# Performance work log

Measured on AMD Instinct MI355X. Metric: run time of the kernel, lower is better.

## Reference

```python
import jax, jax.numpy as jnp
import numpy as np

DIM = 1024
HEAD_DIM = 64
NUM_HEADS = DIM // HEAD_DIM
SCALE = HEAD_DIM ** -0.5
B, N, M = 2, 1024, 2048


def setup_inputs() -> dict:
    key = jax.random.key(0)
    ks = jax.random.split(key, 7)
    x = jax.random.normal(ks[0], (B, N, DIM), dtype=jnp.float32)
    context = jax.random.normal(ks[1], (B, M, DIM), dtype=jnp.float32)
    # query row has at least one valid key (avoids all -inf softmax rows).
    mask = jax.random.bernoulli(ks[2], 0.9, (B, N, M))
    mask = mask.at[:, :, 0].set(True)
    # Linear params (torch nn.Linear convention: y = x @ W.T + b)
    sq = (1.0 / DIM) ** 0.5
    Wq = jax.random.uniform(ks[3], (DIM, DIM), minval=-sq, maxval=sq, dtype=jnp.float32)
    Wkv = jax.random.uniform(ks[4], (2 * DIM, DIM), minval=-sq, maxval=sq, dtype=jnp.float32)
    b_kv = jax.random.uniform(ks[5], (2 * DIM,), minval=-sq, maxval=sq, dtype=jnp.float32)
    Wo = jax.random.uniform(ks[6], (DIM, DIM), minval=-sq, maxval=sq, dtype=jnp.float32)
    return {"x": x, "context": context, "mask": mask,
            "Wq": Wq, "Wkv": Wkv, "b_kv": b_kv, "Wo": Wo}


def reference(x, context, mask, Wq, Wkv, b_kv, Wo):
    b, n, c = x.shape
    m = context.shape[1]
    h, d = NUM_HEADS, HEAD_DIM
    # Q projection (no bias): [b, n, h, d] -> bhnd
    q = (x @ Wq.T).reshape(b, n, h, d).transpose(0, 2, 1, 3)
    # KV projection (with bias): [b, m, 2, h, d]
    kv = (context @ Wkv.T + b_kv).reshape(b, m, 2, h, d)
    k = kv[:, :, 0].transpose(0, 2, 1, 3)  # bhmd
    v = kv[:, :, 1].transpose(0, 2, 1, 3)  # bhmd
    # scores: bhnm, scale applied after matmul as in the original
    attn = jnp.einsum('bhnd,bhmd->bhnm', q, k) * SCALE
    attn = jnp.where(mask[:, None, :, :], attn, -jnp.inf)
    attn = jax.nn.softmax(attn, axis=-1)
    out = jnp.einsum('bhnm,bhmd->bhnd', attn, v)
    out = out.transpose(0, 2, 1, 3).reshape(b, n, h * d)
    return out @ Wo.T
```

## Files before the change

kernel.cpp:

```cpp
#include <hip/hip_runtime.h>


typedef __attribute__((ext_vector_type(8))) short short8;
typedef __attribute__((ext_vector_type(4))) short short4v;
typedef __attribute__((ext_vector_type(4))) float f32x4;
typedef __attribute__((ext_vector_type(4))) int int4v;

#define SCL2E 0.18033688011112042592f

__device__ __forceinline__ float bf2f(short s) {
  unsigned u = ((unsigned)(unsigned short)s) << 16;
  return __uint_as_float(u);
}
__device__ __forceinline__ short f2bf(float f) {
  unsigned u = __float_as_uint(f);
  u += 0x7fffu + ((u >> 16) & 1u);
  return (short)(u >> 16);
}
__device__ __forceinline__ int cvt_pk_bf16(float a, float b) {
  int r;
  asm("v_cvt_pk_bf16_f32 %0, %1, %2" : "=v"(r) : "v"(a), "v"(b));
  return r;
}
__device__ __forceinline__ void gld_lds16(const void* gp, void* lp) {
  __builtin_amdgcn_global_load_lds(
      (const __attribute__((address_space(1))) unsigned int*)gp,
      (__attribute__((address_space(3))) unsigned int*)lp, 16, 0, 0);
}
__device__ __forceinline__ void sbar() {
  __builtin_amdgcn_sched_barrier(0);
  __builtin_amdgcn_s_barrier();
  __builtin_amdgcn_sched_barrier(0);
}
#define WAITVM(N) asm volatile("s_waitcnt vmcnt(" #N ")" ::: "memory")

__device__ __forceinline__ void pipesync() {
  asm volatile("s_waitcnt vmcnt(0) lgkmcnt(0)" ::: "memory");
  __builtin_amdgcn_sched_barrier(0);
  __builtin_amdgcn_s_barrier();
  __builtin_amdgcn_sched_barrier(0);
}
__device__ __forceinline__ short4v cvt4(float4 v) {
  short4v o;
  o[0] = f2bf(v.x); o[1] = f2bf(v.y); o[2] = f2bf(v.z); o[3] = f2bf(v.w);
  return o;
}
__device__ __forceinline__ size_t off128(int row, int k) {
  return ((size_t)(((row >> 7) * 32 + (k >> 5)) * 8 + ((row >> 4) & 7)) << 9) +
         (((((k >> 3) & 3) * 16 + (row & 15)) << 3) + (k & 7));
}
__device__ __forceinline__ size_t off64(int row, int k) {
  return ((size_t)(((row >> 6) * 32 + (k >> 5)) * 4 + ((row >> 4) & 3)) << 9) +
         (((((k >> 3) & 3) * 16 + (row & 15)) << 3) + (k & 7));
}

__global__ __launch_bounds__(256) void prep(
    const unsigned char* __restrict__ mask, unsigned long long* __restrict__ pm,
    const float* __restrict__ Wq, const float* __restrict__ Wkv,
    const float* __restrict__ Wo, const float* __restrict__ x,
    const float* __restrict__ ctx, short* __restrict__ wqb,
    short* __restrict__ wkvb, short* __restrict__ wob,
    short* __restrict__ xb, short* __restrict__ ctxb) {
  const int row = blockIdx.x;
  const int wave = threadIdx.x >> 6, lane = threadIdx.x & 63;
  const unsigned char p8 = mask[lane * 4 + 1];
  const int p32 = ((const int*)mask)[lane * 2 + 1];
  const int shift =
      (__ballot(p8 != 0) != 0ull) ? 0 : ((__ballot(p32 != 0) != 0ull) ? 2 : 3);
  const size_t mbase = ((size_t)row * 2048) << shift;
#pragma unroll
  for (int j = 0; j < 8; j++) {
    const int c = wave * 512 + j * 64 + lane;
    const unsigned long long bits = __ballot(mask[mbase + ((size_t)c << shift)] != 0);
    if (lane == 0) pm[(size_t)row * 32 + wave * 8 + j] = bits;
  }
  const int gid = blockIdx.x * 256 + threadIdx.x;
  {
    const int e = gid * 4, r = e >> 10, k = e & 1023;
    *(short4v*)(xb + off128(r, k)) = cvt4(((const float4*)x)[gid]);
  }
  {
    int e = gid * 4, r = e >> 10, k = e & 1023;
    *(short4v*)(ctxb + off128(r, k)) = cvt4(((const float4*)ctx)[gid]);
    e = (gid + 524288) * 4; r = e >> 10; k = e & 1023;
    *(short4v*)(ctxb + off128(r, k)) = cvt4(((const float4*)ctx)[gid + 524288]);
  }
  {
    const int e = gid * 4, r = e >> 10, k = e & 1023;
    *(short4v*)(wkvb + off128(r, k)) = cvt4(((const float4*)Wkv)[gid]);
  }
  if (gid < 262144) {
    const int e = gid * 4, r = e >> 10, k = e & 1023;
    *(short4v*)(wqb + off128(r, k)) = cvt4(((const float4*)Wq)[gid]);
    *(short4v*)(wob + off64(r, k)) = cvt4(((const float4*)Wo)[gid]);
  }
}

__global__ __launch_bounds__(256, 3)
void qkv_gemm(const short* __restrict__ xb, const short* __restrict__ ctxb,
              const short* __restrict__ wqb, const short* __restrict__ wkvb,
              const float* __restrict__ bias, short* __restrict__ qws,
              short* __restrict__ kws, short* __restrict__ vtws) {
  __shared__ __align__(16) short ldsA[3][4096];
  __shared__ __align__(16) short ldsB[3][4096];
  const int tid = threadIdx.x;
  const int wave = tid >> 6, lane = tid & 63;
  const int l15 = lane & 15, lg = lane >> 4;
  const int bx0 = blockIdx.x;
  const int bx = (bx0 & 7) * 80 + (bx0 >> 3);
  const bool isKV = bx < 512;
  const int rt = isKV ? (bx >> 4) : ((bx - 512) >> 3);
  const int ct = isKV ? (bx & 15) : ((bx - 512) & 7);
  const short* Amat = isKV ? ctxb : xb;
  const short* Bw = isKV ? wkvb : wqb;
  const int wr = wave >> 1, wc = wave & 1;

  f32x4 acc[4][4];
#pragma unroll
  for (int i = 0; i < 4; i++)
#pragma unroll
    for (int j = 0; j < 4; j++) acc[i][j] = (f32x4){0.f, 0.f, 0.f, 0.f};

  const short* ga0 = Amat + (size_t)rt * 131072 + wave * 512 + lane * 8;
  const short* ga1 = ga0 + 2048;
  const short* gb0 = Bw + (size_t)ct * 131072 + wave * 512 + lane * 8;
  const short* gb1 = gb0 + 2048;

  auto stage = [&](int kk, int buf) {
    const size_t koff = (size_t)kk * 4096;
    short* dA = &ldsA[buf][0];
    short* dB = &ldsB[buf][0];
    gld_lds16(ga0 + koff, dA + wave * 512);
    gld_lds16(ga1 + koff, dA + (wave + 4) * 512);
    gld_lds16(gb0 + koff, dB + wave * 512);
    gld_lds16(gb1 + koff, dB + (wave + 4) * 512);
  };
  auto compute = [&](int buf) {
    const short* sA = &ldsA[buf][0];
    const short* sB = &ldsB[buf][0];
    short8 af[4], bfr[4];
#pragma unroll
    for (int t = 0; t < 4; t++)
      af[t] = *(const short8*)&sA[((wr * 4 + t) * 64 + lane) * 8];
#pragma unroll
    for (int t = 0; t < 4; t++)
      bfr[t] = *(const short8*)&sB[((wc * 4 + t) * 64 + lane) * 8];
#pragma unroll
    for (int i = 0; i < 4; i++)
#pragma unroll
      for (int j = 0; j < 4; j++)
        acc[i][j] =
            __builtin_amdgcn_mfma_f32_16x16x32_bf16(af[i], bfr[j], acc[i][j], 0, 0, 0);
  };

  stage(0, 0);
  stage(1, 1);
  int cur = 0, nxt = 2;
  for (int i = 0; i < 30; ++i) {
    WAITVM(4);
    sbar();
    stage(i + 2, nxt);
    compute(cur);
    cur = (cur == 2) ? 0 : cur + 1;
    nxt = (nxt == 2) ? 0 : nxt + 1;
  }
  WAITVM(4);
  sbar();
  compute(cur);
  cur = (cur == 2) ? 0 : cur + 1;
  WAITVM(0);
  sbar();
  compute(cur);

#pragma unroll
  for (int i = 0; i < 4; i++)
#pragma unroll
    for (int j = 0; j < 4; j++)
#pragma unroll
      for (int r = 0; r < 4; r++) {
        const int gr = rt * 128 + wr * 64 + i * 16 + lg * 4 + r;
        const int gc = ct * 128 + wc * 64 + j * 16 + l15;
        float v = acc[i][j][r];
        if (isKV) {
          v += bias[gc];
          const int b = gr >> 11, m = gr & 2047;
          const int kv = gc >> 10, hh = (gc >> 6) & 15, d = gc & 63;
          if (kv == 0)
            kws[((((size_t)b * 16 + hh) * 2048 + m) << 6) + d] = f2bf(v);
          else {
            const int mp = (m & ~31) | (((m >> 2) & 3) << 3) |
                           (((m >> 4) & 1) << 2) | (m & 3);
            vtws[(((size_t)b * 16 + hh) * 64 + d) * 2048 + mp] = f2bf(v);
          }
        } else {
          const int b = gr >> 10, n = gr & 1023, hh = gc >> 6, d = gc & 63;
          qws[((((size_t)b * 16 + hh) * 1024 + n) << 6) + d] = f2bf(v * SCL2E);
        }
      }
}

__global__ __launch_bounds__(512, 4)
void attn_split(const short* __restrict__ Qg, const short* __restrict__ Kg,
                const short* __restrict__ Vtg,
                const unsigned int* __restrict__ pm,
                float* __restrict__ opart, float* __restrict__ lpart) {
  __shared__ __align__(16) short ldsK[2][8192];
  __shared__ __align__(16) short ldsV[2][8192];
  const int tid = threadIdx.x;
  const int w = tid >> 6, lane = tid & 63;
  const int l15 = lane & 15, lg = lane >> 4;
  const int bx = blockIdx.x;
  const int bhid = bx & 31, qt = (bx >> 5) & 7, half = bx >> 8;
  const int b = bhid >> 4, h = bhid & 15;
  const int n0 = qt * 128, m_base = half * 1024;
  const size_t bh = (size_t)b * 16 + h;
  const short* Qb = Qg + (bh * 1024 + n0) * 64;
  const short* Kb = Kg + (bh << 17);
  const short* Vb = Vtg + (bh << 17);
  const unsigned int* pmw =
      pm + ((size_t)(b * 1024 + n0 + w * 16 + l15) << 6) + (m_base >> 5);

  auto stageKV = [&](int c, short* dK, short* dV) {
    const int m0 = m_base + c * 128;
#pragma unroll
    for (int ii = 0; ii < 2; ii++) {
      const int f = w * 2 + ii;
      const int t = f >> 1, ks = f & 1;
      gld_lds16(Kb + (size_t)(m0 + t * 16 + l15) * 64 + ks * 32 + lg * 8,
                dK + f * 512);
      const int vt = f >> 2, vk = f & 3;
      gld_lds16(Vb + (size_t)(vt * 16 + l15) * 2048 + (m0 + vk * 32 + lg * 8),
                dV + f * 512);
    }
  };

#pragma unroll
  for (int ii = 0; ii < 2; ii++)
    gld_lds16(Qb + (size_t)(w * 16 + l15) * 64 + ii * 32 + lg * 8,
              &ldsK[0][(w * 2 + ii) * 512]);
  stageKV(0, ldsK[1], ldsV[1]);
  pipesync();
  short8 qf[2];
#pragma unroll
  for (int ks = 0; ks < 2; ks++)
    qf[ks] = *(const short8*)&ldsK[0][((w * 2 + ks) * 64 + lane) * 8];
  asm volatile("s_waitcnt lgkmcnt(0)" ::: "memory");
  __builtin_amdgcn_sched_barrier(0);
  __builtin_amdgcn_s_barrier();
  __builtin_amdgcn_sched_barrier(0);

  short8 onesf;
#pragma unroll
  for (int i = 0; i < 8; i++) onesf[i] = (short)0x3F80;

  f32x4 o[4], lacc;
#pragma unroll
  for (int ct = 0; ct < 4; ct++) o[ct] = (f32x4){0.f, 0.f, 0.f, 0.f};
  lacc = (f32x4){0.f, 0.f, 0.f, 0.f};
  const int sb = lg * 4;

  auto computeC = [&](int c, const short* sK, const short* sV) {
    const uint4 mk = *(const uint4*)(pmw + c * 4);
    int4v pw4[4];
#pragma unroll
    for (int h2 = 0; h2 < 2; h2++) {
      f32x4 s[4];
#pragma unroll
      for (int t2 = 0; t2 < 4; t2++) s[t2] = (f32x4){0.f, 0.f, 0.f, 0.f};
#pragma unroll
      for (int t2 = 0; t2 < 4; t2++) {
        const int t = h2 * 4 + t2;
#pragma unroll
        for (int ks = 0; ks < 2; ks++) {
          const short8 kf = *(const short8*)&sK[((t * 2 + ks) * 64 + lane) * 8];
          s[t2] = __builtin_amdgcn_mfma_f32_16x16x32_bf16(kf, qf[ks], s[t2], 0, 0, 0);
        }
      }
#pragma unroll
      for (int t2 = 0; t2 < 4; t2++) {
        const int t = h2 * 4 + t2;
        const unsigned int mw = ((t >> 1) == 0) ? mk.x
                              : ((t >> 1) == 1) ? mk.y
                              : ((t >> 1) == 2) ? mk.z : mk.w;
        float p[4];
#pragma unroll
        for (int r = 0; r < 4; r++) {
          const bool att = (mw >> (((t & 1) << 4) + sb + r)) & 1;
          p[r] = exp2f(att ? s[t2][r] : -1e30f);
        }
        pw4[t >> 1][(t & 1) * 2] = cvt_pk_bf16(p[0], p[1]);
        pw4[t >> 1][(t & 1) * 2 + 1] = cvt_pk_bf16(p[2], p[3]);
      }
    }
#pragma unroll
    for (int ks2 = 0; ks2 < 4; ks2++) {
      const short8 pf = __builtin_bit_cast(short8, pw4[ks2]);
#pragma unroll
      for (int ct = 0; ct < 4; ct++) {
        const short8 vf = *(const short8*)&sV[((ct * 4 + ks2) * 64 + lane) * 8];
        o[ct] = __builtin_amdgcn_mfma_f32_16x16x32_bf16(pf, vf, o[ct], 0, 0, 0);
      }
      lacc = __builtin_amdgcn_mfma_f32_16x16x32_bf16(pf, onesf, lacc, 0, 0, 0);
    }
  };

  for (int c = 0; c < 8; c += 2) {
    if (c + 1 < 8) stageKV(c + 1, ldsK[0], ldsV[0]);
    computeC(c, ldsK[1], ldsV[1]);
    pipesync();
    if (c + 2 < 8) stageKV(c + 2, ldsK[1], ldsV[1]);
    computeC(c + 1, ldsK[0], ldsV[0]);
    pipesync();
  }

#pragma unroll
  for (int ct = 0; ct < 4; ct++)
#pragma unroll
    for (int r = 0; r < 4; r++) {
      const int n = n0 + w * 16 + lg * 4 + r;
      opart[((size_t)half << 21) + (((size_t)b * 1024 + n) << 10) + h * 64 +
            ct * 16 + l15] = o[ct][r];
    }
  if (l15 == 0) {
#pragma unroll
    for (int r = 0; r < 4; r++) {
      const int n = n0 + w * 16 + lg * 4 + r;
      lpart[((size_t)half << 15) + bh * 1024 + n] = lacc[r];
    }
  }
}

__global__ __launch_bounds__(256) void combine(
    const float* __restrict__ opart, const float* __restrict__ lpart,
    short* __restrict__ aoT) {
  const int gid = blockIdx.x * 256 + threadIdx.x;
  const size_t base = (size_t)gid * 4;
  const int row = (int)(base >> 10), col = (int)(base & 1023);
  const int b = row >> 10, n = row & 1023, h = col >> 6;
  const float4 o1 = *(const float4*)(opart + base);
  const float4 o2 = *(const float4*)(opart + (1u << 21) + base);
  const float l1 = lpart[(size_t)(b * 16 + h) * 1024 + n];
  const float l2 = lpart[(1u << 15) + (size_t)(b * 16 + h) * 1024 + n];
  const float inv = 1.f / fmaxf(l1 + l2, 1e-30f);
  short4v o;
  o[0] = f2bf((o1.x + o2.x) * inv); o[1] = f2bf((o1.y + o2.y) * inv);
  o[2] = f2bf((o1.z + o2.z) * inv); o[3] = f2bf((o1.w + o2.w) * inv);
  *(short4v*)(aoT + off64(row, col)) = o;
}

__global__ __launch_bounds__(256, 2)
void o_gemm(const short* __restrict__ aoT, const short* __restrict__ wobT,
            float* __restrict__ Of) {
  __shared__ __align__(16) short ldsA[3][2048];
  __shared__ __align__(16) short ldsB[3][2048];
  const int tid = threadIdx.x;
  const int w = tid >> 6, lane = tid & 63;
  const int l15 = lane & 15, lg = lane >> 4;
  const int bx0 = blockIdx.x;
  const int bx = (bx0 & 7) * 64 + (bx0 >> 3);
  const int rt = bx >> 4, ct = bx & 15;

  f32x4 acc[4];
#pragma unroll
  for (int j = 0; j < 4; j++) acc[j] = (f32x4){0.f, 0.f, 0.f, 0.f};

  const short* ga = aoT + (size_t)rt * 65536 + w * 512 + lane * 8;
  const short* gb = wobT + (size_t)ct * 65536 + w * 512 + lane * 8;

  auto stage = [&](int kk, int buf) {
    const size_t koff = (size_t)kk * 2048;
    gld_lds16(ga + koff, &ldsA[buf][0] + w * 512);
    gld_lds16(gb + koff, &ldsB[buf][0] + w * 512);
  };
  auto compute = [&](int buf) {
    const short* sA = &ldsA[buf][0];
    const short* sB = &ldsB[buf][0];
    const short8 af = *(const short8*)&sA[(w * 64 + lane) * 8];
#pragma unroll
    for (int j = 0; j < 4; j++) {
      const short8 bf = *(const short8*)&sB[(j * 64 + lane) * 8];
      acc[j] = __builtin_amdgcn_mfma_f32_16x16x32_bf16(af, bf, acc[j], 0, 0, 0);
    }
  };

  stage(0, 0);
  stage(1, 1);
  int cur = 0, nxt = 2;
  for (int i = 0; i < 30; ++i) {
    WAITVM(2);
    sbar();
    stage(i + 2, nxt);
    compute(cur);
    cur = (cur == 2) ? 0 : cur + 1;
    nxt = (nxt == 2) ? 0 : nxt + 1;
  }
  WAITVM(2);
  sbar();
  compute(cur);
  cur = (cur == 2) ? 0 : cur + 1;
  WAITVM(0);
  sbar();
  compute(cur);

#pragma unroll
  for (int j = 0; j < 4; j++)
#pragma unroll
    for (int r = 0; r < 4; r++) {
      const int gr = rt * 64 + w * 16 + lg * 4 + r;
      const int gc = ct * 64 + j * 16 + l15;
      Of[(size_t)gr * 1024 + gc] = acc[j][r];
    }
}

extern "C" void kernel_launch(void* const* d_in, const int* in_sizes, int n_in,
                              void* d_out, int out_size, void* d_ws, size_t ws_size,
                              hipStream_t stream) {
  const float* x   = (const float*)d_in[0];
  const float* ctx = (const float*)d_in[1];
  const unsigned char* mask = (const unsigned char*)d_in[2];
  const float* Wq  = (const float*)d_in[3];
  const float* Wkv = (const float*)d_in[4];
  const float* bkv = (const float*)d_in[5];
  const float* Wo  = (const float*)d_in[6];
  float* out = (float*)d_out;

  char* wsb = (char*)d_ws;
  short* qws  = (short*)(wsb);
  short* kws  = (short*)(wsb + (4u << 20));
  short* vtws = (short*)(wsb + (12u << 20));
  short* wqb  = (short*)(wsb + (20u << 20));
  short* wkvb = (short*)(wsb + (22u << 20));
  short* wob  = (short*)(wsb + (26u << 20));
  unsigned long long* pmws = (unsigned long long*)(wsb + (28u << 20));
  float* opart = (float*)(wsb + (29u << 20));
  float* lpart = (float*)(wsb + (45u << 20));
  short* xb   = (short*)(wsb + (29u << 20));
  short* ctxb = (short*)(wsb + (33u << 20));
  short* ao = (short*)(wsb + (20u << 20));

  prep<<<2048, 256, 0, stream>>>(mask, pmws, Wq, Wkv, Wo, x, ctx,
                                 wqb, wkvb, wob, xb, ctxb);
  qkv_gemm<<<640, 256, 0, stream>>>(xb, ctxb, wqb, wkvb, bkv, qws, kws, vtws);
  attn_split<<<512, 512, 0, stream>>>(qws, kws, vtws, (const unsigned int*)pmws,
                                      opart, lpart);
  combine<<<2048, 256, 0, stream>>>(opart, lpart, ao);
  o_gemm<<<512, 256, 0, stream>>>(ao, wob, out);
}
```

Baseline: 229.9 us.

## Restructure attention KV pipeline with preloaded masks and deepen O-GEMM k-step

The attention kernel now preloads all eight mask words up front and replaces the two-chunk manual loop with a fully unrolled loop. That loop uses partial vmcnt waits and barriers around each chunk, and Q is moved to a different LDS slot. The output-projection GEMM doubles its k-step per stage, halving the iteration count with two MFMAs per tile, and raises its occupancy hint from 2 to 3. The aim is fewer barriers and loop overheads and better latency hiding. The cost is doubled LDS per block and extra registers for the mask words, which could limit occupancy.

```diff
diff --git a/kernel.cpp b/kernel.cpp
--- a/kernel.cpp
+++ b/kernel.cpp
@@ -220,8 +220,14 @@
   const unsigned int* pmw =
       pm + ((size_t)(b * 1024 + n0 + w * 16 + l15) << 6) + (m_base >> 5);
 
-  auto stageKV = [&](int c, short* dK, short* dV) {
+  uint4 mku[8];
+#pragma unroll
+  for (int c = 0; c < 8; c++) mku[c] = *(const uint4*)(pmw + c * 4);
+
+  auto stageKV = [&](int c, int buf) {
     const int m0 = m_base + c * 128;
+    short* dK = &ldsK[buf][0];
+    short* dV = &ldsV[buf][0];
 #pragma unroll
     for (int ii = 0; ii < 2; ii++) {
       const int f = w * 2 + ii;
@@ -237,17 +243,15 @@
 #pragma unroll
   for (int ii = 0; ii < 2; ii++)
     gld_lds16(Qb + (size_t)(w * 16 + l15) * 64 + ii * 32 + lg * 8,
-              &ldsK[0][(w * 2 + ii) * 512]);
-  stageKV(0, ldsK[1], ldsV[1]);
+              &ldsV[1][(w * 2 + ii) * 512]);
+  stageKV(0, 0);
   pipesync();
   short8 qf[2];
 #pragma unroll
   for (int ks = 0; ks < 2; ks++)
-    qf[ks] = *(const short8*)&ldsK[0][((w * 2 + ks) * 64 + lane) * 8];
+    qf[ks] = *(const short8*)&ldsV[1][((w * 2 + ks) * 64 + lane) * 8];
   asm volatile("s_waitcnt lgkmcnt(0)" ::: "memory");
-  __builtin_amdgcn_sched_barrier(0);
-  __builtin_amdgcn_s_barrier();
-  __builtin_amdgcn_sched_barrier(0);
+  sbar();
 
   short8 onesf;
 #pragma unroll
@@ -259,8 +263,9 @@
   lacc = (f32x4){0.f, 0.f, 0.f, 0.f};
   const int sb = lg * 4;
 
-  auto computeC = [&](int c, const short* sK, const short* sV) {
-    const uint4 mk = *(const uint4*)(pmw + c * 4);
+  auto computeC = [&](uint4 mk, int buf) {
+    const short* sK = &ldsK[buf][0];
+    const short* sV = &ldsV[buf][0];
     int4v pw4[4];
 #pragma unroll
     for (int h2 = 0; h2 < 2; h2++) {
@@ -304,13 +309,17 @@
     }
   };
 
-  for (int c = 0; c < 8; c += 2) {
-    if (c + 1 < 8) stageKV(c + 1, ldsK[0], ldsV[0]);
-    computeC(c, ldsK[1], ldsV[1]);
-    pipesync();
-    if (c + 2 < 8) stageKV(c + 2, ldsK[1], ldsV[1]);
-    computeC(c + 1, ldsK[0], ldsV[0]);
-    pipesync();
+#pragma unroll
+  for (int c = 0; c < 8; c++) {
+    if (c + 1 < 8) {
+      stageKV(c + 1, (c + 1) & 1);
+      WAITVM(4);
+    } else {
+      WAITVM(0);
+    }
+    sbar();
+    computeC(mku[c], c & 1);
+    sbar();
   }
 
 #pragma unroll
@@ -348,11 +357,11 @@
   *(short4v*)(aoT + off64(row, col)) = o;
 }
 
-__global__ __launch_bounds__(256, 2)
+__global__ __launch_bounds__(256, 3)
 void o_gemm(const short* __restrict__ aoT, const short* __restrict__ wobT,
             float* __restrict__ Of) {
-  __shared__ __align__(16) short ldsA[3][2048];
-  __shared__ __align__(16) short ldsB[3][2048];
+  __shared__ __align__(16) short ldsA[3][4096];
+  __shared__ __align__(16) short ldsB[3][4096];
   const int tid = threadIdx.x;
   const int w = tid >> 6, lane = tid & 63;
   const int l15 = lane & 15, lg = lane >> 4;
@@ -367,40 +376,42 @@
   const short* ga = aoT + (size_t)rt * 65536 + w * 512 + lane * 8;
   const short* gb = wobT + (size_t)ct * 65536 + w * 512 + lane * 8;
 
-  auto stage = [&](int kk, int buf) {
-    const size_t koff = (size_t)kk * 2048;
+  auto stage = [&](int t, int buf) {
+    const size_t koff = (size_t)t * 4096;
     gld_lds16(ga + koff, &ldsA[buf][0] + w * 512);
+    gld_lds16(ga + koff + 2048, &ldsA[buf][0] + 2048 + w * 512);
     gld_lds16(gb + koff, &ldsB[buf][0] + w * 512);
+    gld_lds16(gb + koff + 2048, &ldsB[buf][0] + 2048 + w * 512);
   };
   auto compute = [&](int buf) {
     const short* sA = &ldsA[buf][0];
     const short* sB = &ldsB[buf][0];
-    const short8 af = *(const short8*)&sA[(w * 64 + lane) * 8];
+    const short8 af0 = *(const short8*)&sA[(w * 64 + lane) * 8];
+    const short8 af1 = *(const short8*)&sA[2048 + (w * 64 + lane) * 8];
 #pragma unroll
     for (int j = 0; j < 4; j++) {
-      const short8 bf = *(const short8*)&sB[(j * 64 + lane) * 8];
-      acc[j] = __builtin_amdgcn_mfma_f32_16x16x32_bf16(af, bf, acc[j], 0, 0, 0);
+      const short8 bf0 = *(const short8*)&sB[(j * 64 + lane) * 8];
+      const short8 bf1 = *(const short8*)&sB[2048 + (j * 64 + lane) * 8];
+      acc[j] = __builtin_amdgcn_mfma_f32_16x16x32_bf16(af0, bf0, acc[j], 0, 0, 0);
+      acc[j] = __builtin_amdgcn_mfma_f32_16x16x32_bf16(af1, bf1, acc[j], 0, 0, 0);
     }
   };
 
   stage(0, 0);
   stage(1, 1);
-  int cur = 0, nxt = 2;
-  for (int i = 0; i < 30; ++i) {
-    WAITVM(2);
+#pragma unroll
+  for (int i = 0; i < 14; ++i) {
+    WAITVM(4);
     sbar();
-    stage(i + 2, nxt);
-    compute(cur);
-    cur = (cur == 2) ? 0 : cur + 1;
-    nxt = (nxt == 2) ? 0 : nxt + 1;
-  }
-  WAITVM(2);
+    stage(i + 2, (i + 2) % 3);
+    compute(i % 3);
+  }
+  WAITVM(4);
   sbar();
-  compute(cur);
-  cur = (cur == 2) ? 0 : cur + 1;
+  compute(14 % 3);
   WAITVM(0);
   sbar();
-  compute(cur);
+  compute(15 % 3);
 
 #pragma unroll
   for (int j = 0; j < 4; j++)
```

After: 221.8 us. 3.5% less time.
